# Optimization experiments

Hardware: AMD Instinct MI355X
Metric: run time of the kernel (lower is better)

The kernel has to match this reference:

```python
import jax, jax.numpy as jnp
import numpy as np

N_NODES = 100000
N_EDGES = 3200000
N_GRAPHS = 1000

def setup_inputs() -> dict:
    key = jax.random.key(0)
    ks = jax.random.split(key, 8)
    x = jax.random.normal(ks[0], (N_NODES, 4), dtype=jnp.float32)
    edge_index = jax.random.randint(ks[1], (2, N_EDGES), 0, N_NODES, dtype=jnp.int64)
    batch = jnp.sort(jax.random.randint(ks[2], (N_NODES,), 0, N_GRAPHS, dtype=jnp.int64))
    def glorot(k, shape):
        lim = np.sqrt(6.0 / (shape[0] + shape[1]))
        return jax.random.uniform(k, shape, jnp.float32, -lim, lim)
    return {
        'x': x, 'edge_index': edge_index, 'batch': batch,
        'W1': glorot(ks[3], (4, 16)),  'b1': jnp.zeros((16,), jnp.float32),
        'W2': glorot(ks[4], (16, 16)), 'b2': jnp.zeros((16,), jnp.float32),
        'W3': glorot(ks[5], (16, 16)), 'b3': jnp.zeros((16,), jnp.float32),
        'lin_w': glorot(ks[6], (16, 1)), 'lin_b': jnp.zeros((1,), jnp.float32),
    }

def _gcn_norm(edge_index, num_nodes):
    # PyG GCNConv default: add self-loops, symmetric normalization
    loop = jnp.arange(num_nodes, dtype=edge_index.dtype)
    row = jnp.concatenate([edge_index[0], loop])  # source
    col = jnp.concatenate([edge_index[1], loop])  # target
    ones = jnp.ones(row.shape[0], dtype=jnp.float32)
    deg = jax.ops.segment_sum(ones, col, num_segments=num_nodes)
    dinv = jnp.where(deg > 0, jax.lax.rsqrt(deg), 0.0)
    norm = dinv[row] * dinv[col]  # [E+N]
    return row, col, norm

def _gcn_conv(x, row, col, norm, W, b, num_nodes):
    h = x @ W                                   # small GEMM first (fewer msg bytes)
    msg = h[row] * norm[:, None]                # gather + scale
    out = jax.ops.segment_sum(msg, col, num_segments=num_nodes)  # scatter-add
    return out + b

def reference(x, edge_index, batch, W1, b1, W2, b2, W3, b3, lin_w, lin_b):
    n = x.shape[0]
    row, col, norm = _gcn_norm(edge_index, n)
    h = _gcn_conv(x, row, col, norm, W1, b1, n)
    h = _gcn_conv(h, row, col, norm, W2, b2, n)
    h = _gcn_conv(h, row, col, norm, W3, b3, n)
    # global_mean_pool
    sums = jax.ops.segment_sum(h, batch, num_segments=N_GRAPHS)
    cnt = jax.ops.segment_sum(jnp.ones((n,), jnp.float32), batch, num_segments=N_GRAPHS)
    pooled = sums / jnp.maximum(cnt, 1.0)[:, None]
    # dropout p=0.5 is identity in eval mode
    logits = pooled @ lin_w + lin_b
    return jax.nn.sigmoid(logits)
```

## Files before the change

kernel.cpp:

```cpp
#include <hip/hip_runtime.h>
#include <math.h>


#define SHIFT      8
#define BSZ        256
#define NB_SCAT    256
#define B_SCAT     1024
#define B_GATH     1024
#define ROWMASK    0x1FFFFu
#define PSLOTS     64
#define MAXNB      2048

__global__ void hist_kernel(const int* __restrict__ col, int E, int tile, int nbuck,
                            unsigned* __restrict__ M,
                            const float* __restrict__ W1, const float* __restrict__ b1,
                            const float* __restrict__ W2, const float* __restrict__ b2,
                            const float* __restrict__ W3, const float* __restrict__ b3,
                            const float* __restrict__ lin_w, const float* __restrict__ lin_b,
                            float* __restrict__ coeff,
                            float* __restrict__ sums, float* __restrict__ cnt, int ngraphs) {
    extern __shared__ unsigned h[];
    __shared__ float w3l[16], w2l[16];
    int t = threadIdx.x;
    for (int i = t; i < nbuck; i += blockDim.x) h[i] = 0;
    if (blockIdx.x == 0) {
        for (int i = t; i < ngraphs; i += blockDim.x) { sums[i] = 0.f; cnt[i] = 0.f; }
        if (t < 16) {
            float s = 0.f;
            for (int j = 0; j < 16; ++j) s += W3[t * 16 + j] * lin_w[j];
            w3l[t] = s;
        }
    }
    __syncthreads();
    if (blockIdx.x == 0 && t < 16) {
        float s = 0.f;
        for (int j = 0; j < 16; ++j) s += W2[t * 16 + j] * w3l[j];
        w2l[t] = s;
    }
    __syncthreads();
    if (blockIdx.x == 0) {
        if (t < 4) {
            float s = 0.f;
            for (int j = 0; j < 16; ++j) s += W1[t * 16 + j] * w2l[j];
            coeff[t] = s;
        } else if (t == 4) {
            float s = 0.f;
            for (int j = 0; j < 16; ++j) s += b1[j] * w2l[j];
            coeff[4] = s;
        } else if (t == 5) {
            float s = 0.f;
            for (int j = 0; j < 16; ++j) s += b2[j] * w3l[j];
            coeff[5] = s;
        } else if (t == 6) {
            float s = 0.f;
            for (int j = 0; j < 16; ++j) s += b3[j] * lin_w[j];
            coeff[6] = s;
        } else if (t == 7) {
            coeff[7] = lin_b[0];
        }
    }
    int b = blockIdx.x;
    int s = b * tile, e = min(s + tile, E);
    if (s < e) {
        int nq = (e - s) >> 2;
        const int4* c4 = (const int4*)(col + s);
        for (int q = t; q < nq; q += blockDim.x) {
            int4 c = c4[q];
            atomicAdd(&h[((unsigned)c.x) >> SHIFT], 1u);
            atomicAdd(&h[((unsigned)c.y) >> SHIFT], 1u);
            atomicAdd(&h[((unsigned)c.z) >> SHIFT], 1u);
            atomicAdd(&h[((unsigned)c.w) >> SHIFT], 1u);
        }
        for (int k = s + (nq << 2) + t; k < e; k += blockDim.x)
            atomicAdd(&h[((unsigned)col[k]) >> SHIFT], 1u);
    }
    __syncthreads();
    for (int i = t; i < nbuck; i += blockDim.x)
        M[(size_t)b * nbuck + i] = h[i];
}

__global__ void scanA_kernel(unsigned* __restrict__ M, unsigned* __restrict__ binTotal,
                             int nbuck) {
    __shared__ unsigned sc[NB_SCAT];
    int b = blockIdx.x;
    int t = threadIdx.x;
    unsigned v = M[(size_t)t * nbuck + b];
    sc[t] = v;
    __syncthreads();
    for (int off = 1; off < NB_SCAT; off <<= 1) {
        unsigned u = (t >= off) ? sc[t - off] : 0u;
        __syncthreads();
        sc[t] += u;
        __syncthreads();
    }
    M[(size_t)t * nbuck + b] = sc[t] - v;
    if (t == NB_SCAT - 1) binTotal[b] = sc[t];
}

__global__ void scatter_kernel(const int* __restrict__ row, const int* __restrict__ col,
                               int E, int tile, int nbuck,
                               const unsigned* __restrict__ M,
                               const unsigned* __restrict__ binTotal,
                               unsigned* __restrict__ bstart,
                               unsigned* __restrict__ out) {
    extern __shared__ unsigned lds[];
    unsigned* h     = lds;
    unsigned* lofs  = lds + nbuck;
    unsigned* lcur  = lds + 2 * nbuck;
    unsigned* gbase = lds + 3 * nbuck;
    unsigned* tsum  = lds + 4 * nbuck;
    unsigned* stage = lds + 4 * nbuck + B_SCAT;
    int t = threadIdx.x, j = blockIdx.x;
    for (int i = t; i < nbuck; i += blockDim.x) h[i] = 0;
    __syncthreads();
    int s = j * tile, e = min(s + tile, E);
    if (s < e) {
        int nq = (e - s) >> 2;
        const int4* c4 = (const int4*)(col + s);
        for (int q = t; q < nq; q += blockDim.x) {
            int4 c = c4[q];
            atomicAdd(&h[((unsigned)c.x) >> SHIFT], 1u);
            atomicAdd(&h[((unsigned)c.y) >> SHIFT], 1u);
            atomicAdd(&h[((unsigned)c.z) >> SHIFT], 1u);
            atomicAdd(&h[((unsigned)c.w) >> SHIFT], 1u);
        }
        for (int k = s + (nq << 2) + t; k < e; k += blockDim.x)
            atomicAdd(&h[((unsigned)col[k]) >> SHIFT], 1u);
    }
    __syncthreads();
    const int C = MAXNB / B_SCAT;
    unsigned lv[C];
    {
        unsigned run = 0;
        for (int k = 0; k < C; ++k) {
            int i = t * C + k;
            unsigned x = (i < nbuck) ? h[i] : 0u;
            lv[k] = run; run += x;
        }
        tsum[t] = run;
        __syncthreads();
        for (int off = 1; off < B_SCAT; off <<= 1) {
            unsigned u = (t >= off) ? tsum[t - off] : 0u;
            __syncthreads();
            tsum[t] += u;
            __syncthreads();
        }
        unsigned ex = (t == 0) ? 0u : tsum[t - 1];
        for (int k = 0; k < C; ++k) {
            int i = t * C + k;
            if (i < nbuck) { lofs[i] = ex + lv[k]; lcur[i] = ex + lv[k]; }
        }
    }
    __syncthreads();
    {
        unsigned run = 0;
        for (int k = 0; k < C; ++k) {
            int i = t * C + k;
            unsigned x = (i < nbuck) ? binTotal[i] : 0u;
            lv[k] = run; run += x;
        }
        tsum[t] = run;
        __syncthreads();
        for (int off = 1; off < B_SCAT; off <<= 1) {
            unsigned u = (t >= off) ? tsum[t - off] : 0u;
            __syncthreads();
            tsum[t] += u;
            __syncthreads();
        }
        unsigned ex = (t == 0) ? 0u : tsum[t - 1];
        for (int k = 0; k < C; ++k) {
            int i = t * C + k;
            if (i < nbuck) {
                unsigned bb = ex + lv[k];
                gbase[i] = bb + M[(size_t)j * nbuck + i];
                if (j == 0) bstart[i] = bb;
            }
        }
        if (j == 0 && t == 0) bstart[nbuck] = (unsigned)E;
    }
    __syncthreads();
    if (s < e) {
        int nq = (e - s) >> 2;
        const int4* r4 = (const int4*)(row + s);
        const int4* c4 = (const int4*)(col + s);
        for (int q = t; q < nq; q += blockDim.x) {
            int4 r = r4[q];
            int4 c = c4[q];
            unsigned p0 = atomicAdd(&lcur[((unsigned)c.x) >> SHIFT], 1u);
            unsigned p1 = atomicAdd(&lcur[((unsigned)c.y) >> SHIFT], 1u);
            unsigned p2 = atomicAdd(&lcur[((unsigned)c.z) >> SHIFT], 1u);
            unsigned p3 = atomicAdd(&lcur[((unsigned)c.w) >> SHIFT], 1u);
            stage[p0] = (unsigned)r.x | (((unsigned)c.x & (BSZ - 1)) << 17);
            stage[p1] = (unsigned)r.y | (((unsigned)c.y & (BSZ - 1)) << 17);
            stage[p2] = (unsigned)r.z | (((unsigned)c.z & (BSZ - 1)) << 17);
            stage[p3] = (unsigned)r.w | (((unsigned)c.w & (BSZ - 1)) << 17);
        }
        for (int k = s + (nq << 2) + t; k < e; k += blockDim.x) {
            unsigned c = (unsigned)col[k];
            unsigned pos = atomicAdd(&lcur[c >> SHIFT], 1u);
            stage[pos] = (unsigned)row[k] | ((c & (BSZ - 1)) << 17);
        }
    }
    __syncthreads();
    int wid = t >> 6, lane = t & 63, nw = blockDim.x >> 6;
    for (int b = wid; b < nbuck; b += nw) {
        unsigned cntb = h[b], lo = lofs[b], go = gbase[b];
        for (unsigned i = lane; i < cntb; i += 64)
            out[go + i] = stage[lo + i];
    }
}

__global__ void degnode0_kernel(const unsigned* __restrict__ buck,
                                const unsigned* __restrict__ bstart,
                                const float* __restrict__ x, const float* __restrict__ coeff,
                                float* __restrict__ dinv, float* __restrict__ g, int n) {
    __shared__ float acc[BSZ];
    int b = blockIdx.x;
    if (threadIdx.x < BSZ) acc[threadIdx.x] = 0.f;
    __syncthreads();
    unsigned s = bstart[b], e = bstart[b + 1];
    unsigned sa = (s + 3u) & ~3u;
    if (sa > e) sa = e;
    if (s + threadIdx.x < sa)
        atomicAdd(&acc[buck[s + threadIdx.x] >> 17], 1.0f);
    unsigned nq = (e - sa) >> 2;
    const uint4* bq = (const uint4*)(buck + sa);
    for (unsigned q = threadIdx.x; q < nq; q += blockDim.x) {
        uint4 w = bq[q];
        atomicAdd(&acc[w.x >> 17], 1.0f);
        atomicAdd(&acc[w.y >> 17], 1.0f);
        atomicAdd(&acc[w.z >> 17], 1.0f);
        atomicAdd(&acc[w.w >> 17], 1.0f);
    }
    for (unsigned k = sa + (nq << 2) + threadIdx.x; k < e; k += blockDim.x)
        atomicAdd(&acc[buck[k] >> 17], 1.0f);
    __syncthreads();
    int node = b * BSZ + threadIdx.x;
    if (threadIdx.x < BSZ && node < n) {
        float d = rsqrtf(acc[threadIdx.x] + 1.0f);
        dinv[node] = d;
        float4 xv = ((const float4*)x)[node];
        float t0 = xv.x * coeff[0] + xv.y * coeff[1] + xv.z * coeff[2] + xv.w * coeff[3];
        g[node] = d * t0;
    }
}

__global__ void gather_kernel(const unsigned* __restrict__ buck,
                              const unsigned* __restrict__ bstart,
                              const float* __restrict__ dinv, const float* __restrict__ gin,
                              float* __restrict__ gout, const float* __restrict__ coeff,
                              int sidx, int n) {
    __shared__ float acc[BSZ];
    int b = blockIdx.x;
    if (threadIdx.x < BSZ) acc[threadIdx.x] = 0.f;
    __syncthreads();
    unsigned s = bstart[b], e = bstart[b + 1];
    unsigned sa = (s + 3u) & ~3u;
    if (sa > e) sa = e;
    if (s + threadIdx.x < sa) {
        unsigned w = buck[s + threadIdx.x];
        atomicAdd(&acc[w >> 17], gin[w & ROWMASK]);
    }
    unsigned nq = (e - sa) >> 2;
    const uint4* bq = (const uint4*)(buck + sa);
    for (unsigned q = threadIdx.x; q < nq; q += blockDim.x) {
        uint4 w = bq[q];
        float a0 = gin[w.x & ROWMASK];
        float a1 = gin[w.y & ROWMASK];
        float a2 = gin[w.z & ROWMASK];
        float a3 = gin[w.w & ROWMASK];
        atomicAdd(&acc[w.x >> 17], a0);
        atomicAdd(&acc[w.y >> 17], a1);
        atomicAdd(&acc[w.z >> 17], a2);
        atomicAdd(&acc[w.w >> 17], a3);
    }
    for (unsigned k = sa + (nq << 2) + threadIdx.x; k < e; k += blockDim.x) {
        unsigned w = buck[k];
        atomicAdd(&acc[w >> 17], gin[w & ROWMASK]);
    }
    __syncthreads();
    int node = b * BSZ + threadIdx.x;
    if (threadIdx.x < BSZ && node < n) {
        float d = dinv[node];
        float t = d * (acc[threadIdx.x] + gin[node]) + coeff[sidx];
        gout[node] = d * t;
    }
}

__global__ void gatherpool_kernel(const unsigned* __restrict__ buck,
                                  const unsigned* __restrict__ bstart,
                                  const float* __restrict__ dinv, const float* __restrict__ gin,
                                  const float* __restrict__ coeff, const int* __restrict__ batch,
                                  float* __restrict__ sums, float* __restrict__ cnt, int n) {
    __shared__ float acc[BSZ];
    __shared__ float ls[PSLOTS], lc[PSLOTS];
    __shared__ int bF;
    int b = blockIdx.x;
    if (threadIdx.x < BSZ) acc[threadIdx.x] = 0.f;
    for (int i = threadIdx.x; i < PSLOTS; i += blockDim.x) { ls[i] = 0.f; lc[i] = 0.f; }
    if (threadIdx.x == 0) bF = batch[min(b * BSZ, n - 1)];
    __syncthreads();
    unsigned s = bstart[b], e = bstart[b + 1];
    unsigned sa = (s + 3u) & ~3u;
    if (sa > e) sa = e;
    if (s + threadIdx.x < sa) {
        unsigned w = buck[s + threadIdx.x];
        atomicAdd(&acc[w >> 17], gin[w & ROWMASK]);
    }
    unsigned nq = (e - sa) >> 2;
    const uint4* bq = (const uint4*)(buck + sa);
    for (unsigned q = threadIdx.x; q < nq; q += blockDim.x) {
        uint4 w = bq[q];
        float a0 = gin[w.x & ROWMASK];
        float a1 = gin[w.y & ROWMASK];
        float a2 = gin[w.z & ROWMASK];
        float a3 = gin[w.w & ROWMASK];
        atomicAdd(&acc[w.x >> 17], a0);
        atomicAdd(&acc[w.y >> 17], a1);
        atomicAdd(&acc[w.z >> 17], a2);
        atomicAdd(&acc[w.w >> 17], a3);
    }
    for (unsigned k = sa + (nq << 2) + threadIdx.x; k < e; k += blockDim.x) {
        unsigned w = buck[k];
        atomicAdd(&acc[w >> 17], gin[w & ROWMASK]);
    }
    __syncthreads();
    int node = b * BSZ + threadIdx.x;
    if (threadIdx.x < BSZ && node < n) {
        float d = dinv[node];
        float t3 = d * (acc[threadIdx.x] + gin[node]) + coeff[6];
        int rb = batch[node] - bF;
        if (rb < PSLOTS) {
            atomicAdd(&ls[rb], t3);
            atomicAdd(&lc[rb], 1.0f);
        } else {
            atomicAdd(&sums[bF + rb], t3);
            atomicAdd(&cnt[bF + rb], 1.0f);
        }
    }
    __syncthreads();
    for (int i = threadIdx.x; i < PSLOTS; i += blockDim.x) {
        if (lc[i] != 0.f) {
            atomicAdd(&sums[bF + i], ls[i]);
            atomicAdd(&cnt[bF + i], lc[i]);
        }
    }
}

__global__ void final_kernel(const float* __restrict__ sums, const float* __restrict__ cnt,
                             const float* __restrict__ coeff, float* __restrict__ out,
                             int ngraphs) {
    int i = blockIdx.x * blockDim.x + threadIdx.x;
    if (i < ngraphs) {
        float m = sums[i] / fmaxf(cnt[i], 1.0f) + coeff[7];
        out[i] = 1.0f / (1.0f + expf(-m));
    }
}

__global__ void fb_coeffs_kernel(const float* __restrict__ W1, const float* __restrict__ b1,
                                 const float* __restrict__ W2, const float* __restrict__ b2,
                                 const float* __restrict__ W3, const float* __restrict__ b3,
                                 const float* __restrict__ lin_w, const float* __restrict__ lin_b,
                                 float* __restrict__ coeff,
                                 float* __restrict__ sums, float* __restrict__ cnt, int ngraphs) {
    for (int i = threadIdx.x; i < ngraphs; i += blockDim.x) { sums[i] = 0.f; cnt[i] = 0.f; }
    if (threadIdx.x == 0) {
        float w3l[16], w2l[16];
        for (int i = 0; i < 16; ++i) {
            float s = 0.f;
            for (int j = 0; j < 16; ++j) s += W3[i * 16 + j] * lin_w[j];
            w3l[i] = s;
        }
        for (int i = 0; i < 16; ++i) {
            float s = 0.f;
            for (int j = 0; j < 16; ++j) s += W2[i * 16 + j] * w3l[j];
            w2l[i] = s;
        }
        for (int i = 0; i < 4; ++i) {
            float s = 0.f;
            for (int j = 0; j < 16; ++j) s += W1[i * 16 + j] * w2l[j];
            coeff[i] = s;
        }
        float s2 = 0.f, s1 = 0.f, s0 = 0.f;
        for (int j = 0; j < 16; ++j) {
            s2 += b1[j] * w2l[j];
            s1 += b2[j] * w3l[j];
            s0 += b3[j] * lin_w[j];
        }
        coeff[4] = s2; coeff[5] = s1; coeff[6] = s0; coeff[7] = lin_b[0];
    }
}
__global__ void fb_init_kernel(float* __restrict__ deg, int n) {
    int i = blockIdx.x * blockDim.x + threadIdx.x;
    int stride = gridDim.x * blockDim.x;
    for (int k = i; k < n; k += stride) deg[k] = 1.0f;
}
__global__ void fb_deg_kernel(const int* __restrict__ col, float* __restrict__ deg, int E) {
    int i = blockIdx.x * blockDim.x + threadIdx.x;
    int stride = gridDim.x * blockDim.x;
    for (int k = i; k < E; k += stride) atomicAdd(&deg[col[k]], 1.0f);
}
__global__ void fb_node0_kernel(const float* __restrict__ x, const float* __restrict__ coeff,
                                float* __restrict__ deg_dinv, float* __restrict__ g,
                                float* __restrict__ acc, int n) {
    int i = blockIdx.x * blockDim.x + threadIdx.x;
    int stride = gridDim.x * blockDim.x;
    for (int k = i; k < n; k += stride) {
        float d = rsqrtf(deg_dinv[k]);
        deg_dinv[k] = d;
        float4 xv = ((const float4*)x)[k];
        float t0 = xv.x * coeff[0] + xv.y * coeff[1] + xv.z * coeff[2] + xv.w * coeff[3];
        g[k] = d * t0;
        acc[k] = 0.f;
    }
}
__global__ void fb_edge_kernel(const int* __restrict__ ei, const float* __restrict__ g,
                               float* __restrict__ acc, int E) {
    int i = blockIdx.x * blockDim.x + threadIdx.x;
    int stride = gridDim.x * blockDim.x;
    for (int k = i; k < E; k += stride) atomicAdd(&acc[ei[E + k]], g[ei[k]]);
}
__global__ void fb_node_kernel(const float* __restrict__ dinv, float* __restrict__ g,
                               float* __restrict__ acc, const float* __restrict__ coeff,
                               int sidx, int n) {
    int i = blockIdx.x * blockDim.x + threadIdx.x;
    int stride = gridDim.x * blockDim.x;
    for (int k = i; k < n; k += stride) {
        float d = dinv[k];
        float t = d * (acc[k] + g[k]) + coeff[sidx];
        g[k] = d * t;
        acc[k] = 0.f;
    }
}
__global__ void fb_pool_kernel(const float* __restrict__ dinv, const float* __restrict__ g,
                               const float* __restrict__ acc, const float* __restrict__ coeff,
                               const int* __restrict__ batch, float* __restrict__ sums,
                               float* __restrict__ cnt, int n) {
    int i = blockIdx.x * blockDim.x + threadIdx.x;
    int stride = gridDim.x * blockDim.x;
    for (int k = i; k < n; k += stride) {
        float d = dinv[k];
        float t3 = d * (acc[k] + g[k]) + coeff[6];
        int b = batch[k];
        atomicAdd(&sums[b], t3);
        atomicAdd(&cnt[b], 1.0f);
    }
}

extern "C" void kernel_launch(void* const* d_in, const int* in_sizes, int n_in,
                              void* d_out, int out_size, void* d_ws, size_t ws_size,
                              hipStream_t stream) {
    const float* x     = (const float*)d_in[0];
    const int*   ei    = (const int*)d_in[1];
    const int*   batch = (const int*)d_in[2];
    const float* W1    = (const float*)d_in[3];
    const float* b1    = (const float*)d_in[4];
    const float* W2    = (const float*)d_in[5];
    const float* b2    = (const float*)d_in[6];
    const float* W3    = (const float*)d_in[7];
    const float* b3    = (const float*)d_in[8];
    const float* lin_w = (const float*)d_in[9];
    const float* lin_b = (const float*)d_in[10];

    const int n       = in_sizes[0] / 4;
    const int E       = in_sizes[1] / 2;
    const int ngraphs = out_size;

    const int nbuck = (n + BSZ - 1) / BSZ;
    const int B = 256;

    size_t npad  = ((size_t)n + 255) & ~(size_t)255;
    size_t gpad  = ((size_t)ngraphs + 255) & ~(size_t)255;
    size_t nbpad = ((size_t)nbuck + 1 + 255) & ~(size_t)255;
    size_t mlen  = (size_t)NB_SCAT * nbuck;

    size_t need = (256 + mlen + 2 * nbpad + (size_t)E + 3 * npad + 2 * gpad) * 4;

    float* ws    = (float*)d_ws;
    float* coeff = ws;
    unsigned* M        = (unsigned*)(coeff + 256);
    unsigned* binTotal = M + mlen;
    unsigned* bstart   = binTotal + nbpad;
    unsigned* buck     = bstart + nbpad;
    float* dinv  = (float*)(buck + E);
    float* gA    = dinv + npad;
    float* gB    = gA + npad;
    float* sums  = gB + npad;
    float* cnt   = sums + gpad;

    int tile = (((E + NB_SCAT - 1) / NB_SCAT) + 3) & ~3;
    size_t ldsScat = (size_t)(4 * nbuck + B_SCAT + tile) * sizeof(unsigned);

    bool mainok = (n < (1 << 17)) && nbuck >= 1 && nbuck <= MAXNB &&
                  ws_size >= need && ldsScat <= 63 * 1024;

    if (!mainok) {
        float* fcoeff = ws;
        float* deg = fcoeff + 256;
        float* g   = deg + npad;
        float* acc = g + npad;
        float* fsums = acc + npad;
        float* fcnt  = fsums + gpad;
        int nodeBlocks = (n + B - 1) / B;
        int edgeBlocks = (E + B - 1) / B;
        fb_coeffs_kernel<<<1, 64, 0, stream>>>(W1, b1, W2, b2, W3, b3, lin_w, lin_b, fcoeff,
                                               fsums, fcnt, ngraphs);
        fb_init_kernel<<<nodeBlocks, B, 0, stream>>>(deg, n);
        fb_deg_kernel<<<edgeBlocks, B, 0, stream>>>(ei + E, deg, E);
        fb_node0_kernel<<<nodeBlocks, B, 0, stream>>>(x, fcoeff, deg, g, acc, n);
        fb_edge_kernel<<<edgeBlocks, B, 0, stream>>>(ei, g, acc, E);
        fb_node_kernel<<<nodeBlocks, B, 0, stream>>>(deg, g, acc, fcoeff, 4, n);
        fb_edge_kernel<<<edgeBlocks, B, 0, stream>>>(ei, g, acc, E);
        fb_node_kernel<<<nodeBlocks, B, 0, stream>>>(deg, g, acc, fcoeff, 5, n);
        fb_edge_kernel<<<edgeBlocks, B, 0, stream>>>(ei, g, acc, E);
        fb_pool_kernel<<<nodeBlocks, B, 0, stream>>>(deg, g, acc, fcoeff, batch, fsums, fcnt, n);
        final_kernel<<<(ngraphs + B - 1) / B, B, 0, stream>>>(fsums, fcnt, fcoeff, (float*)d_out, ngraphs);
        return;
    }

    size_t ldsHist = (size_t)nbuck * sizeof(unsigned);

    hist_kernel<<<NB_SCAT, B_SCAT, ldsHist, stream>>>(ei + E, E, tile, nbuck, M,
                                                      W1, b1, W2, b2, W3, b3, lin_w, lin_b,
                                                      coeff, sums, cnt, ngraphs);
    scanA_kernel<<<nbuck, NB_SCAT, 0, stream>>>(M, binTotal, nbuck);
    scatter_kernel<<<NB_SCAT, B_SCAT, ldsScat, stream>>>(ei, ei + E, E, tile, nbuck, M,
                                                         binTotal, bstart, buck);

    degnode0_kernel<<<nbuck, B_GATH, 0, stream>>>(buck, bstart, x, coeff, dinv, gA, n);
    gather_kernel<<<nbuck, B_GATH, 0, stream>>>(buck, bstart, dinv, gA, gB, coeff, 4, n);
    gather_kernel<<<nbuck, B_GATH, 0, stream>>>(buck, bstart, dinv, gB, gA, coeff, 5, n);
    gatherpool_kernel<<<nbuck, B_GATH, 0, stream>>>(buck, bstart, dinv, gA, coeff, batch,
                                                    sums, cnt, n);

    final_kernel<<<(ngraphs + B - 1) / B, B, 0, stream>>>(sums, cnt, coeff, (float*)d_out, ngraphs);
}
```

Measured before the change: 129.4 us.

## Fuse gather phases into cooperative mega-kernel and reuse histogram in scatter

```diff
diff --git a/kernel.cpp b/kernel.cpp
--- a/kernel.cpp
+++ b/kernel.cpp
@@ -1,4 +1,5 @@
 #include <hip/hip_runtime.h>
+#include <hip/hip_cooperative_groups.h>
 #include <math.h>
 
 
@@ -6,13 +7,15 @@
 #define BSZ        256
 #define NB_SCAT    256
 #define B_SCAT     1024
-#define B_GATH     1024
+#define B_MEGA     1024
 #define ROWMASK    0x1FFFFu
 #define PSLOTS     64
 #define MAXNB      2048
 
+namespace cg = cooperative_groups;
+
 __global__ void hist_kernel(const int* __restrict__ col, int E, int tile, int nbuck,
-                            unsigned* __restrict__ M,
+                            unsigned* __restrict__ Mcnt, unsigned* __restrict__ Mloc,
                             const float* __restrict__ W1, const float* __restrict__ b1,
                             const float* __restrict__ W2, const float* __restrict__ b2,
                             const float* __restrict__ W3, const float* __restrict__ b3,
@@ -20,6 +23,7 @@
                             float* __restrict__ coeff,
                             float* __restrict__ sums, float* __restrict__ cnt, int ngraphs) {
     extern __shared__ unsigned h[];
+    __shared__ unsigned tsum[B_SCAT];
     __shared__ float w3l[16], w2l[16];
     int t = threadIdx.x;
     for (int i = t; i < nbuck; i += blockDim.x) h[i] = 0;
@@ -75,16 +79,38 @@
             atomicAdd(&h[((unsigned)col[k]) >> SHIFT], 1u);
     }
     __syncthreads();
-    for (int i = t; i < nbuck; i += blockDim.x)
-        M[(size_t)b * nbuck + i] = h[i];
-}
-
-__global__ void scanA_kernel(unsigned* __restrict__ M, unsigned* __restrict__ binTotal,
-                             int nbuck) {
+    const int C = MAXNB / B_SCAT;
+    unsigned lv[C];
+    unsigned run = 0;
+    for (int k = 0; k < C; ++k) {
+        int i = t * C + k;
+        unsigned x = (i < nbuck) ? h[i] : 0u;
+        lv[k] = run; run += x;
+    }
+    tsum[t] = run;
+    __syncthreads();
+    for (int off = 1; off < B_SCAT; off <<= 1) {
+        unsigned u = (t >= off) ? tsum[t - off] : 0u;
+        __syncthreads();
+        tsum[t] += u;
+        __syncthreads();
+    }
+    unsigned ex = (t == 0) ? 0u : tsum[t - 1];
+    for (int k = 0; k < C; ++k) {
+        int i = t * C + k;
+        if (i < nbuck) {
+            Mcnt[(size_t)b * nbuck + i] = h[i];
+            Mloc[(size_t)b * nbuck + i] = ex + lv[k];
+        }
+    }
+}
+
+__global__ void scanA_kernel(const unsigned* __restrict__ Mcnt, unsigned* __restrict__ Mpre,
+                             unsigned* __restrict__ binTotal, int nbuck) {
     __shared__ unsigned sc[NB_SCAT];
     int b = blockIdx.x;
     int t = threadIdx.x;
-    unsigned v = M[(size_t)t * nbuck + b];
+    unsigned v = Mcnt[(size_t)t * nbuck + b];
     sc[t] = v;
     __syncthreads();
     for (int off = 1; off < NB_SCAT; off <<= 1) {
@@ -93,92 +119,59 @@
         sc[t] += u;
         __syncthreads();
     }
-    M[(size_t)t * nbuck + b] = sc[t] - v;
+    Mpre[(size_t)t * nbuck + b] = sc[t] - v;
     if (t == NB_SCAT - 1) binTotal[b] = sc[t];
 }
 
 __global__ void scatter_kernel(const int* __restrict__ row, const int* __restrict__ col,
                                int E, int tile, int nbuck,
-                               const unsigned* __restrict__ M,
+                               const unsigned* __restrict__ Mcnt,
+                               const unsigned* __restrict__ Mloc,
+                               const unsigned* __restrict__ Mpre,
                                const unsigned* __restrict__ binTotal,
                                unsigned* __restrict__ bstart,
                                unsigned* __restrict__ out) {
     extern __shared__ unsigned lds[];
-    unsigned* h     = lds;
+    unsigned* hA    = lds;
     unsigned* lofs  = lds + nbuck;
     unsigned* lcur  = lds + 2 * nbuck;
     unsigned* gbase = lds + 3 * nbuck;
     unsigned* tsum  = lds + 4 * nbuck;
     unsigned* stage = lds + 4 * nbuck + B_SCAT;
     int t = threadIdx.x, j = blockIdx.x;
-    for (int i = t; i < nbuck; i += blockDim.x) h[i] = 0;
-    __syncthreads();
-    int s = j * tile, e = min(s + tile, E);
-    if (s < e) {
-        int nq = (e - s) >> 2;
-        const int4* c4 = (const int4*)(col + s);
-        for (int q = t; q < nq; q += blockDim.x) {
-            int4 c = c4[q];
-            atomicAdd(&h[((unsigned)c.x) >> SHIFT], 1u);
-            atomicAdd(&h[((unsigned)c.y) >> SHIFT], 1u);
-            atomicAdd(&h[((unsigned)c.z) >> SHIFT], 1u);
-            atomicAdd(&h[((unsigned)c.w) >> SHIFT], 1u);
-        }
-        for (int k = s + (nq << 2) + t; k < e; k += blockDim.x)
-            atomicAdd(&h[((unsigned)col[k]) >> SHIFT], 1u);
-    }
-    __syncthreads();
+    for (int i = t; i < nbuck; i += blockDim.x) {
+        unsigned c = Mcnt[(size_t)j * nbuck + i];
+        unsigned l = Mloc[(size_t)j * nbuck + i];
+        hA[i] = c; lofs[i] = l; lcur[i] = l;
+    }
     const int C = MAXNB / B_SCAT;
     unsigned lv[C];
-    {
-        unsigned run = 0;
-        for (int k = 0; k < C; ++k) {
-            int i = t * C + k;
-            unsigned x = (i < nbuck) ? h[i] : 0u;
-            lv[k] = run; run += x;
-        }
-        tsum[t] = run;
+    unsigned run = 0;
+    for (int k = 0; k < C; ++k) {
+        int i = t * C + k;
+        unsigned x = (i < nbuck) ? binTotal[i] : 0u;
+        lv[k] = run; run += x;
+    }
+    tsum[t] = run;
+    __syncthreads();
+    for (int off = 1; off < B_SCAT; off <<= 1) {
+        unsigned u = (t >= off) ? tsum[t - off] : 0u;
         __syncthreads();
-        for (int off = 1; off < B_SCAT; off <<= 1) {
-            unsigned u = (t >= off) ? tsum[t - off] : 0u;
-            __syncthreads();
-            tsum[t] += u;
-            __syncthreads();
-        }
-        unsigned ex = (t == 0) ? 0u : tsum[t - 1];
-        for (int k = 0; k < C; ++k) {
-            int i = t * C + k;
-            if (i < nbuck) { lofs[i] = ex + lv[k]; lcur[i] = ex + lv[k]; }
-        }
-    }
-    __syncthreads();
-    {
-        unsigned run = 0;
-        for (int k = 0; k < C; ++k) {
-            int i = t * C + k;
-            unsigned x = (i < nbuck) ? binTotal[i] : 0u;
-            lv[k] = run; run += x;
-        }
-        tsum[t] = run;
+        tsum[t] += u;
         __syncthreads();
-        for (int off = 1; off < B_SCAT; off <<= 1) {
-            unsigned u = (t >= off) ? tsum[t - off] : 0u;
-            __syncthreads();
-            tsum[t] += u;
-            __syncthreads();
-        }
-        unsigned ex = (t == 0) ? 0u : tsum[t - 1];
-        for (int k = 0; k < C; ++k) {
-            int i = t * C + k;
-            if (i < nbuck) {
-                unsigned bb = ex + lv[k];
-                gbase[i] = bb + M[(size_t)j * nbuck + i];
-                if (j == 0) bstart[i] = bb;
-            }
-        }
-        if (j == 0 && t == 0) bstart[nbuck] = (unsigned)E;
-    }
-    __syncthreads();
+    }
+    unsigned ex = (t == 0) ? 0u : tsum[t - 1];
+    for (int k = 0; k < C; ++k) {
+        int i = t * C + k;
+        if (i < nbuck) {
+            unsigned bb = ex + lv[k];
+            gbase[i] = bb + Mpre[(size_t)j * nbuck + i];
+            if (j == 0) bstart[i] = bb;
+        }
+    }
+    if (j == 0 && t == 0) bstart[nbuck] = (unsigned)E;
+    __syncthreads();
+    int s = j * tile, e = min(s + tile, E);
     if (s < e) {
         int nq = (e - s) >> 2;
         const int4* r4 = (const int4*)(row + s);
@@ -204,21 +197,44 @@
     __syncthreads();
     int wid = t >> 6, lane = t & 63, nw = blockDim.x >> 6;
     for (int b = wid; b < nbuck; b += nw) {
-        unsigned cntb = h[b], lo = lofs[b], go = gbase[b];
+        unsigned cntb = hA[b], lo = lofs[b], go = gbase[b];
         for (unsigned i = lane; i < cntb; i += 64)
             out[go + i] = stage[lo + i];
     }
 }
 
-__global__ void degnode0_kernel(const unsigned* __restrict__ buck,
-                                const unsigned* __restrict__ bstart,
-                                const float* __restrict__ x, const float* __restrict__ coeff,
-                                float* __restrict__ dinv, float* __restrict__ g, int n) {
-    __shared__ float acc[BSZ];
-    int b = blockIdx.x;
-    if (threadIdx.x < BSZ) acc[threadIdx.x] = 0.f;
-    __syncthreads();
-    unsigned s = bstart[b], e = bstart[b + 1];
+__device__ __forceinline__ void accum_gather(const unsigned* __restrict__ buck,
+                                             unsigned s, unsigned e,
+                                             const float* __restrict__ gin,
+                                             float* __restrict__ acc) {
+    unsigned sa = (s + 3u) & ~3u;
+    if (sa > e) sa = e;
+    if (s + threadIdx.x < sa) {
+        unsigned w = buck[s + threadIdx.x];
+        atomicAdd(&acc[w >> 17], gin[w & ROWMASK]);
+    }
+    unsigned nq = (e - sa) >> 2;
+    const uint4* bq = (const uint4*)(buck + sa);
+    for (unsigned q = threadIdx.x; q < nq; q += blockDim.x) {
+        uint4 w = bq[q];
+        float a0 = gin[w.x & ROWMASK];
+        float a1 = gin[w.y & ROWMASK];
+        float a2 = gin[w.z & ROWMASK];
+        float a3 = gin[w.w & ROWMASK];
+        atomicAdd(&acc[w.x >> 17], a0);
+        atomicAdd(&acc[w.y >> 17], a1);
+        atomicAdd(&acc[w.z >> 17], a2);
+        atomicAdd(&acc[w.w >> 17], a3);
+    }
+    for (unsigned k = sa + (nq << 2) + threadIdx.x; k < e; k += blockDim.x) {
+        unsigned w = buck[k];
+        atomicAdd(&acc[w >> 17], gin[w & ROWMASK]);
+    }
+}
+
+__device__ __forceinline__ void accum_count(const unsigned* __restrict__ buck,
+                                            unsigned s, unsigned e,
+                                            float* __restrict__ acc) {
     unsigned sa = (s + 3u) & ~3u;
     if (sa > e) sa = e;
     if (s + threadIdx.x < sa)
@@ -234,101 +250,67 @@
     }
     for (unsigned k = sa + (nq << 2) + threadIdx.x; k < e; k += blockDim.x)
         atomicAdd(&acc[buck[k] >> 17], 1.0f);
-    __syncthreads();
-    int node = b * BSZ + threadIdx.x;
-    if (threadIdx.x < BSZ && node < n) {
-        float d = rsqrtf(acc[threadIdx.x] + 1.0f);
+}
+
+__global__ __launch_bounds__(B_MEGA, 8)
+void mega_kernel(const unsigned* __restrict__ buck, const unsigned* __restrict__ bstart,
+                 const float* __restrict__ x, const float* __restrict__ coeff,
+                 const int* __restrict__ batch,
+                 float* __restrict__ dinv, float* __restrict__ gA, float* __restrict__ gB,
+                 float* __restrict__ sums, float* __restrict__ cnt,
+                 float* __restrict__ out, int n, int nbuck, int ngraphs) {
+    cg::grid_group grid = cg::this_grid();
+    __shared__ float acc[BSZ];
+    __shared__ float ls[PSLOTS], lc[PSLOTS];
+    __shared__ int bF;
+    int b = blockIdx.x, t = threadIdx.x;
+    unsigned s = bstart[b], e = bstart[b + 1];
+    int node = b * BSZ + t;
+
+    if (t < BSZ) acc[t] = 0.f;
+    __syncthreads();
+    accum_count(buck, s, e, acc);
+    __syncthreads();
+    if (t < BSZ && node < n) {
+        float d = rsqrtf(acc[t] + 1.0f);
         dinv[node] = d;
         float4 xv = ((const float4*)x)[node];
         float t0 = xv.x * coeff[0] + xv.y * coeff[1] + xv.z * coeff[2] + xv.w * coeff[3];
-        g[node] = d * t0;
-    }
-}
-
-__global__ void gather_kernel(const unsigned* __restrict__ buck,
-                              const unsigned* __restrict__ bstart,
-                              const float* __restrict__ dinv, const float* __restrict__ gin,
-                              float* __restrict__ gout, const float* __restrict__ coeff,
-                              int sidx, int n) {
-    __shared__ float acc[BSZ];
-    int b = blockIdx.x;
-    if (threadIdx.x < BSZ) acc[threadIdx.x] = 0.f;
-    __syncthreads();
-    unsigned s = bstart[b], e = bstart[b + 1];
-    unsigned sa = (s + 3u) & ~3u;
-    if (sa > e) sa = e;
-    if (s + threadIdx.x < sa) {
-        unsigned w = buck[s + threadIdx.x];
-        atomicAdd(&acc[w >> 17], gin[w & ROWMASK]);
-    }
-    unsigned nq = (e - sa) >> 2;
-    const uint4* bq = (const uint4*)(buck + sa);
-    for (unsigned q = threadIdx.x; q < nq; q += blockDim.x) {
-        uint4 w = bq[q];
-        float a0 = gin[w.x & ROWMASK];
-        float a1 = gin[w.y & ROWMASK];
-        float a2 = gin[w.z & ROWMASK];
-        float a3 = gin[w.w & ROWMASK];
-        atomicAdd(&acc[w.x >> 17], a0);
-        atomicAdd(&acc[w.y >> 17], a1);
-        atomicAdd(&acc[w.z >> 17], a2);
-        atomicAdd(&acc[w.w >> 17], a3);
-    }
-    for (unsigned k = sa + (nq << 2) + threadIdx.x; k < e; k += blockDim.x) {
-        unsigned w = buck[k];
-        atomicAdd(&acc[w >> 17], gin[w & ROWMASK]);
-    }
-    __syncthreads();
-    int node = b * BSZ + threadIdx.x;
-    if (threadIdx.x < BSZ && node < n) {
+        gA[node] = d * t0;
+    }
+    grid.sync();
+
+    if (t < BSZ) acc[t] = 0.f;
+    __syncthreads();
+    accum_gather(buck, s, e, gA, acc);
+    __syncthreads();
+    if (t < BSZ && node < n) {
         float d = dinv[node];
-        float t = d * (acc[threadIdx.x] + gin[node]) + coeff[sidx];
-        gout[node] = d * t;
-    }
-}
-
-__global__ void gatherpool_kernel(const unsigned* __restrict__ buck,
-                                  const unsigned* __restrict__ bstart,
-                                  const float* __restrict__ dinv, const float* __restrict__ gin,
-                                  const float* __restrict__ coeff, const int* __restrict__ batch,
-                                  float* __restrict__ sums, float* __restrict__ cnt, int n) {
-    __shared__ float acc[BSZ];
-    __shared__ float ls[PSLOTS], lc[PSLOTS];
-    __shared__ int bF;
-    int b = blockIdx.x;
-    if (threadIdx.x < BSZ) acc[threadIdx.x] = 0.f;
-    for (int i = threadIdx.x; i < PSLOTS; i += blockDim.x) { ls[i] = 0.f; lc[i] = 0.f; }
-    if (threadIdx.x == 0) bF = batch[min(b * BSZ, n - 1)];
-    __syncthreads();
-    unsigned s = bstart[b], e = bstart[b + 1];
-    unsigned sa = (s + 3u) & ~3u;
-    if (sa > e) sa = e;
-    if (s + threadIdx.x < sa) {
-        unsigned w = buck[s + threadIdx.x];
-        atomicAdd(&acc[w >> 17], gin[w & ROWMASK]);
-    }
-    unsigned nq = (e - sa) >> 2;
-    const uint4* bq = (const uint4*)(buck + sa);
-    for (unsigned q = threadIdx.x; q < nq; q += blockDim.x) {
-        uint4 w = bq[q];
-        float a0 = gin[w.x & ROWMASK];
-        float a1 = gin[w.y & ROWMASK];
-        float a2 = gin[w.z & ROWMASK];
-        float a3 = gin[w.w & ROWMASK];
-        atomicAdd(&acc[w.x >> 17], a0);
-        atomicAdd(&acc[w.y >> 17], a1);
-        atomicAdd(&acc[w.z >> 17], a2);
-        atomicAdd(&acc[w.w >> 17], a3);
-    }
-    for (unsigned k = sa + (nq << 2) + threadIdx.x; k < e; k += blockDim.x) {
-        unsigned w = buck[k];
-        atomicAdd(&acc[w >> 17], gin[w & ROWMASK]);
-    }
-    __syncthreads();
-    int node = b * BSZ + threadIdx.x;
-    if (threadIdx.x < BSZ && node < n) {
+        float tt = d * (acc[t] + gA[node]) + coeff[4];
+        gB[node] = d * tt;
+    }
+    grid.sync();
+
+    if (t < BSZ) acc[t] = 0.f;
+    __syncthreads();
+    accum_gather(buck, s, e, gB, acc);
+    __syncthreads();
+    if (t < BSZ && node < n) {
         float d = dinv[node];
-        float t3 = d * (acc[threadIdx.x] + gin[node]) + coeff[6];
+        float tt = d * (acc[t] + gB[node]) + coeff[5];
+        gA[node] = d * tt;
+    }
+    grid.sync();
+
+    if (t < BSZ) acc[t] = 0.f;
+    for (int i = t; i < PSLOTS; i += blockDim.x) { ls[i] = 0.f; lc[i] = 0.f; }
+    if (t == 0) bF = batch[min(b * BSZ, n - 1)];
+    __syncthreads();
+    accum_gather(buck, s, e, gA, acc);
+    __syncthreads();
+    if (t < BSZ && node < n) {
+        float d = dinv[node];
+        float t3 = d * (acc[t] + gA[node]) + coeff[6];
         int rb = batch[node] - bF;
         if (rb < PSLOTS) {
             atomicAdd(&ls[rb], t3);
@@ -339,21 +321,19 @@
         }
     }
     __syncthreads();
-    for (int i = threadIdx.x; i < PSLOTS; i += blockDim.x) {
+    for (int i = t; i < PSLOTS; i += blockDim.x) {
         if (lc[i] != 0.f) {
             atomicAdd(&sums[bF + i], ls[i]);
             atomicAdd(&cnt[bF + i], lc[i]);
         }
     }
-}
-
-__global__ void final_kernel(const float* __restrict__ sums, const float* __restrict__ cnt,
-                             const float* __restrict__ coeff, float* __restrict__ out,
-                             int ngraphs) {
-    int i = blockIdx.x * blockDim.x + threadIdx.x;
-    if (i < ngraphs) {
-        float m = sums[i] / fmaxf(cnt[i], 1.0f) + coeff[7];
-        out[i] = 1.0f / (1.0f + expf(-m));
+    grid.sync();
+
+    if (b == 0) {
+        for (int i = t; i < ngraphs; i += blockDim.x) {
+            float m = sums[i] / fmaxf(cnt[i], 1.0f) + coeff[7];
+            out[i] = 1.0f / (1.0f + expf(-m));
+        }
     }
 }
 
@@ -444,6 +424,15 @@
         int b = batch[k];
         atomicAdd(&sums[b], t3);
         atomicAdd(&cnt[b], 1.0f);
+    }
+}
+__global__ void fb_final_kernel(const float* __restrict__ sums, const float* __restrict__ cnt,
+                                const float* __restrict__ coeff, float* __restrict__ out,
+                                int ngraphs) {
+    int i = blockIdx.x * blockDim.x + threadIdx.x;
+    if (i < ngraphs) {
+        float m = sums[i] / fmaxf(cnt[i], 1.0f) + coeff[7];
+        out[i] = 1.0f / (1.0f + expf(-m));
     }
 }
 
@@ -474,12 +463,14 @@
     size_t nbpad = ((size_t)nbuck + 1 + 255) & ~(size_t)255;
     size_t mlen  = (size_t)NB_SCAT * nbuck;
 
-    size_t need = (256 + mlen + 2 * nbpad + (size_t)E + 3 * npad + 2 * gpad) * 4;
+    size_t need = (256 + 3 * mlen + 2 * nbpad + (size_t)E + 3 * npad + 2 * gpad) * 4;
 
     float* ws    = (float*)d_ws;
     float* coeff = ws;
-    unsigned* M        = (unsigned*)(coeff + 256);
-    unsigned* binTotal = M + mlen;
+    unsigned* Mcnt     = (unsigned*)(coeff + 256);
+    unsigned* Mloc     = Mcnt + mlen;
+    unsigned* Mpre     = Mloc + mlen;
+    unsigned* binTotal = Mpre + mlen;
     unsigned* bstart   = binTotal + nbpad;
     unsigned* buck     = bstart + nbpad;
     float* dinv  = (float*)(buck + E);
@@ -491,7 +482,7 @@
     int tile = (((E + NB_SCAT - 1) / NB_SCAT) + 3) & ~3;
     size_t ldsScat = (size_t)(4 * nbuck + B_SCAT + tile) * sizeof(unsigned);
 
-    bool mainok = (n < (1 << 17)) && nbuck >= 1 && nbuck <= MAXNB &&
+    bool mainok = (n < (1 << 17)) && nbuck >= 1 && nbuck <= 512 &&
                   ws_size >= need && ldsScat <= 63 * 1024;
 
     if (!mainok) {
@@ -514,24 +505,25 @@
         fb_node_kernel<<<nodeBlocks, B, 0, stream>>>(deg, g, acc, fcoeff, 5, n);
         fb_edge_kernel<<<edgeBlocks, B, 0, stream>>>(ei, g, acc, E);
         fb_pool_kernel<<<nodeBlocks, B, 0, stream>>>(deg, g, acc, fcoeff, batch, fsums, fcnt, n);
-        final_kernel<<<(ngraphs + B - 1) / B, B, 0, stream>>>(fsums, fcnt, fcoeff, (float*)d_out, ngraphs);
+        fb_final_kernel<<<(ngraphs + B - 1) / B, B, 0, stream>>>(fsums, fcnt, fcoeff, (float*)d_out, ngraphs);
         return;
     }
 
     size_t ldsHist = (size_t)nbuck * sizeof(unsigned);
 
-    hist_kernel<<<NB_SCAT, B_SCAT, ldsHist, stream>>>(ei + E, E, tile, nbuck, M,
+    hist_kernel<<<NB_SCAT, B_SCAT, ldsHist, stream>>>(ei + E, E, tile, nbuck, Mcnt, Mloc,
                                                       W1, b1, W2, b2, W3, b3, lin_w, lin_b,
                                                       coeff, sums, cnt, ngraphs);
-    scanA_kernel<<<nbuck, NB_SCAT, 0, stream>>>(M, binTotal, nbuck);
-    scatter_kernel<<<NB_SCAT, B_SCAT, ldsScat, stream>>>(ei, ei + E, E, tile, nbuck, M,
-                                                         binTotal, bstart, buck);
-
-    degnode0_kernel<<<nbuck, B_GATH, 0, stream>>>(buck, bstart, x, coeff, dinv, gA, n);
-    gather_kernel<<<nbuck, B_GATH, 0, stream>>>(buck, bstart, dinv, gA, gB, coeff, 4, n);
-    gather_kernel<<<nbuck, B_GATH, 0, stream>>>(buck, bstart, dinv, gB, gA, coeff, 5, n);
-    gatherpool_kernel<<<nbuck, B_GATH, 0, stream>>>(buck, bstart, dinv, gA, coeff, batch,
-                                                    sums, cnt, n);
-
-    final_kernel<<<(ngraphs + B - 1) / B, B, 0, stream>>>(sums, cnt, coeff, (float*)d_out, ngraphs);
-}
+    scanA_kernel<<<nbuck, NB_SCAT, 0, stream>>>(Mcnt, Mpre, binTotal, nbuck);
+    scatter_kernel<<<NB_SCAT, B_SCAT, ldsScat, stream>>>(ei, ei + E, E, tile, nbuck,
+                                                         Mcnt, Mloc, Mpre, binTotal,
+                                                         bstart, buck);
+
+    float* outp = (float*)d_out;
+    int n_ = n, nbuck_ = nbuck, ngraphs_ = ngraphs;
+    void* args[] = { (void*)&buck, (void*)&bstart, (void*)&x, (void*)&coeff, (void*)&batch,
+                     (void*)&dinv, (void*)&gA, (void*)&gB, (void*)&sums, (void*)&cnt,
+                     (void*)&outp, (void*)&n_, (void*)&nbuck_, (void*)&ngraphs_ };
+    hipLaunchCooperativeKernel((void*)mega_kernel, dim3(nbuck), dim3(B_MEGA),
+                               args, 0, stream);
+}
```

Result: slower. 290.3 us (+124.4%).
